# Kernel optimization log

Measured on AMD Instinct MI355X. Metric: run time of the kernel, lower is better.

Reference implementation:

```python
import jax, jax.numpy as jnp
import numpy as np

NDIM = 8
P = NDIM * (NDIM - 1) // 2  # 28 upper-triangular pairs
NHIDDEN = 128
NLAYERS = 3  # first layer + (NLAYERS-1) hidden layers, all followed by softplus
BATCH = 65536


def _pair_indices():
    # torch code iterates j outer, i inner, keeping i < j (i >= j skipped)
    pairs = [(i, j) for j in range(NDIM) for i in range(NDIM) if i < j]
    rel = np.array([[k for k in range(NDIM) if k != i and k != j] for (i, j) in pairs],
                   dtype=np.int32)  # [P, NDIM-2]
    i_idx = np.array([p[0] for p in pairs], dtype=np.int32)
    j_idx = np.array([p[1] for p in pairs], dtype=np.int32)
    return rel, i_idx, j_idx


def setup_inputs() -> dict:
    key = jax.random.key(0)
    ks = jax.random.split(key, 7)
    rel, i_idx, j_idx = _pair_indices()
    d_in = NDIM - 2
    x = jax.random.normal(ks[0], (BATCH, NDIM), dtype=jnp.float32)
    # stacked per-pair MLP parameters (kaiming-ish scale)
    W1 = jax.random.normal(ks[1], (P, d_in, NHIDDEN), dtype=jnp.float32) / np.sqrt(d_in)
    b1 = jax.random.normal(ks[2], (P, NHIDDEN), dtype=jnp.float32) * 0.05
    Wh = jax.random.normal(ks[3], (NLAYERS - 1, P, NHIDDEN, NHIDDEN), dtype=jnp.float32) / np.sqrt(NHIDDEN)
    bh = jax.random.normal(ks[4], (NLAYERS - 1, P, NHIDDEN), dtype=jnp.float32) * 0.05
    Wout = jax.random.normal(ks[5], (P, NHIDDEN), dtype=jnp.float32) / np.sqrt(NHIDDEN)
    bout = jax.random.normal(ks[6], (P,), dtype=jnp.float32) * 0.05
    return {
        "x": x, "W1": W1, "b1": b1, "Wh": Wh, "bh": bh,
        "Wout": Wout, "bout": bout,
        "rel_idx": jnp.asarray(rel), "i_idx": jnp.asarray(i_idx), "j_idx": jnp.asarray(j_idx),
    }


def reference(x, W1, b1, Wh, bh, Wout, bout, rel_idx, i_idx, j_idx):
    # gather the ndim-2 relevant coords for every pair: [B, P, NDIM-2]
    xg = x[:, rel_idx]
    # first linear + softplus (batched over the P pairs)
    h = jax.nn.softplus(jnp.einsum('bpd,pdh->bph', xg, W1) + b1)
    # hidden linears + softplus
    for l in range(Wh.shape[0]):
        h = jax.nn.softplus(jnp.einsum('bph,phk->bpk', h, Wh[l]) + bh[l])
    # output head (no activation): scalar per pair -> [B, P]
    vals = jnp.einsum('bph,ph->bp', h, Wout) + bout
    # scatter into upper triangle, then antisymmetrize
    B = x.shape[0]
    J = jnp.zeros((B, NDIM, NDIM), dtype=x.dtype).at[:, i_idx, j_idx].set(vals)
    return J - jnp.swapaxes(J, 1, 2)
```

## Files before the change

### kernel.cpp

```cpp
#include <hip/hip_runtime.h>

#define NDIM 8
#define P_PAIRS 28
#define HID 128
#define BATCH_N 65536
#define TILE_M 256
#define THREADS 512
#define TILES_PER_BLOCK 4

#define LOG2E 1.4426950408889634f
#define LN2   0.6931471805599453f

typedef __attribute__((ext_vector_type(8))) short bf16x8;
typedef __attribute__((ext_vector_type(4))) float f32x4;

__device__ __forceinline__ unsigned short f32_to_bf16(float f) {
  union { float f; unsigned u; } v; v.f = f;
  unsigned r = v.u + 0x7FFFu + ((v.u >> 16) & 1u);
  return (unsigned short)(r >> 16);
}

__device__ __forceinline__ unsigned cvt_pk_bf16(float a, float b) {
  unsigned r;
  asm("v_cvt_pk_bf16_f32 %0, %1, %2" : "=v"(r) : "v"(a), "v"(b));
  return r;
}

__device__ __forceinline__ float fast_exp2(float x) {
  float r; asm("v_exp_f32 %0, %1" : "=v"(r) : "v"(x)); return r;
}
__device__ __forceinline__ float fast_log2(float x) {
  float r; asm("v_log_f32 %0, %1" : "=v"(r) : "v"(x)); return r;
}

__device__ __forceinline__ float softplus2(float t) {
  t = fminf(t, 126.0f);
  return fast_log2(1.0f + fast_exp2(t));
}

__device__ __forceinline__ int swz(int r, int c8) {
  return r * 128 + (((c8 ^ (r & 15)) & 15) << 3);
}

__global__ void prep_wt(const float* __restrict__ Wh, unsigned short* __restrict__ WT) {
  __shared__ float tile[32][33];
  int t = blockIdx.x;
  int lp = t >> 4;
  int sub = t & 15;
  int kt = (sub >> 2) * 32, nt = (sub & 3) * 32;
  const float* src = Wh + (size_t)lp * 16384;
  unsigned short* dst = WT + (size_t)lp * 16384;
  int tx = threadIdx.x & 31, ty = threadIdx.x >> 5;
#pragma unroll
  for (int r = 0; r < 32; r += 8)
    tile[r + ty][tx] = src[(kt + r + ty) * 128 + (nt + tx)];
  __syncthreads();
#pragma unroll
  for (int r = 0; r < 32; r += 8)
    dst[(nt + r + ty) * 128 + (kt + tx)] = f32_to_bf16(tile[tx][r + ty]);
}

__launch_bounds__(THREADS, 2)
__global__ void mlp_pairs(const float* __restrict__ x,
                          const float* __restrict__ W1,
                          const float* __restrict__ b1,
                          const float* __restrict__ bh,
                          const float* __restrict__ Wout,
                          const float* __restrict__ bout,
                          const int* __restrict__ rel_idx,
                          const int* __restrict__ i_idx,
                          const int* __restrict__ j_idx,
                          const unsigned short* __restrict__ WT,
                          float* __restrict__ out) {
  const int p = blockIdx.y;
  const int bx = blockIdx.x;
  const int tid = (int)threadIdx.x;
  const int lane = tid & 63;
  const int wave = tid >> 6;
  const int qd = lane >> 4;
  const int ln = lane & 15;
  const int mrow = wave * 32;

  __shared__ __align__(16) unsigned short w0_lds[128 * 128];
  __shared__ __align__(16) unsigned short w1_lds[128 * 128];
  __shared__ __align__(16) unsigned short h_lds[TILE_M * 128];
  __shared__ __align__(16) unsigned short xg_lds[TILE_M][8];
  __shared__ __align__(16) unsigned short w1t_lds[128][8];
  __shared__ __align__(16) float b1s[128];
  __shared__ __align__(16) float bh0s[128];
  __shared__ __align__(16) float bh1s[128];
  __shared__ __align__(16) float wouts[128];

  {
    const uint4* s0 = reinterpret_cast<const uint4*>(WT + (size_t)p * 16384);
    const uint4* s1 = reinterpret_cast<const uint4*>(WT + (size_t)(P_PAIRS + p) * 16384);
#pragma unroll
    for (int it = 0; it < 4; ++it) {
      int idx = it * THREADS + tid;
      int r = idx >> 4, c = idx & 15;
      uint4 a = s0[idx];
      uint4 b = s1[idx];
      int off = swz(r, c);
      *reinterpret_cast<uint4*>(&w0_lds[off]) = a;
      *reinterpret_cast<uint4*>(&w1_lds[off]) = b;
    }
  }
  if (tid < 128) {
    int n = tid;
    unsigned short u[8];
#pragma unroll
    for (int k = 0; k < 6; ++k)
      u[k] = f32_to_bf16(W1[(p * 6 + k) * 128 + n] * LOG2E);
    u[6] = 0; u[7] = 0;
    uint4 pk;
    pk.x = (unsigned)u[0] | ((unsigned)u[1] << 16);
    pk.y = (unsigned)u[2] | ((unsigned)u[3] << 16);
    pk.z = (unsigned)u[4] | ((unsigned)u[5] << 16);
    pk.w = 0u;
    *reinterpret_cast<uint4*>(&w1t_lds[n][0]) = pk;
  } else if (tid < 256) {
    int n = tid - 128;
    b1s[n]  = b1[p * 128 + n] * LOG2E;
    bh0s[n] = bh[p * 128 + n] * LOG2E;
    bh1s[n] = bh[(P_PAIRS + p) * 128 + n] * LOG2E;
    wouts[n] = Wout[p * 128 + n] * LN2;
  }
  int rl[6];
#pragma unroll
  for (int d = 0; d < 6; ++d) rl[d] = rel_idx[p * 6 + d];
  const int ii = i_idx[p], jj = j_idx[p];
  const float bp = bout[p];
  __syncthreads();

  float4 xa, xb;
  {
    int row = bx * (TILE_M * TILES_PER_BLOCK) + mrow + (lane & 31);
    const float4* xr = reinterpret_cast<const float4*>(x + (size_t)row * 8);
    if (lane < 32) { xa = xr[0]; xb = xr[1]; }
  }

  for (int itile = 0; itile < TILES_PER_BLOCK; ++itile) {
    const int row0 = bx * (TILE_M * TILES_PER_BLOCK) + itile * TILE_M;

    if (lane < 32) {
      int r = mrow + lane;
      float xv[8] = {xa.x, xa.y, xa.z, xa.w, xb.x, xb.y, xb.z, xb.w};
      unsigned short u[8];
#pragma unroll
      for (int d = 0; d < 6; ++d)
        u[d] = f32_to_bf16(xv[rl[d]]);
      u[6] = 0; u[7] = 0;
      uint4 pk;
      pk.x = (unsigned)u[0] | ((unsigned)u[1] << 16);
      pk.y = (unsigned)u[2] | ((unsigned)u[3] << 16);
      pk.z = (unsigned)u[4] | ((unsigned)u[5] << 16);
      pk.w = 0u;
      *reinterpret_cast<uint4*>(&xg_lds[r][0]) = pk;
    }
    if (itile + 1 < TILES_PER_BLOCK && lane < 32) {
      int row = row0 + TILE_M + mrow + (lane & 31);
      const float4* xr = reinterpret_cast<const float4*>(x + (size_t)row * 8);
      xa = xr[0]; xb = xr[1];
    }

    f32x4 acc[2][8];

#pragma unroll
    for (int nt = 0; nt < 8; ++nt) {
      f32x4 b4 = *reinterpret_cast<const f32x4*>(&b1s[nt * 16 + qd * 4]);
      acc[0][nt] = b4;
      acc[1][nt] = b4;
    }
    {
      bf16x8 zero8 = {};
      bf16x8 bfr[2];
#pragma unroll
      for (int mt = 0; mt < 2; ++mt) {
        bfr[mt] = zero8;
        if (qd == 0)
          bfr[mt] = *reinterpret_cast<const bf16x8*>(&xg_lds[mrow + mt * 16 + ln][0]);
      }
#pragma unroll
      for (int nt = 0; nt < 8; ++nt) {
        bf16x8 afr = zero8;
        if (qd == 0)
          afr = *reinterpret_cast<const bf16x8*>(&w1t_lds[nt * 16 + ln][0]);
#pragma unroll
        for (int mt = 0; mt < 2; ++mt)
          acc[mt][nt] = __builtin_amdgcn_mfma_f32_16x16x32_bf16(afr, bfr[mt], acc[mt][nt], 0, 0, 0);
      }
    }
#pragma unroll
    for (int mt = 0; mt < 2; ++mt) {
      int m = mrow + mt * 16 + ln;
#pragma unroll
      for (int nt = 0; nt < 8; ++nt) {
        uint2 pk;
        pk.x = cvt_pk_bf16(softplus2(acc[mt][nt][0]), softplus2(acc[mt][nt][1]));
        pk.y = cvt_pk_bf16(softplus2(acc[mt][nt][2]), softplus2(acc[mt][nt][3]));
        int off = swz(m, nt * 2 + (qd >> 1)) + (qd & 1) * 4;
        *reinterpret_cast<uint2*>(&h_lds[off]) = pk;
      }
    }

#pragma unroll
    for (int nt = 0; nt < 8; ++nt) {
      f32x4 b4 = *reinterpret_cast<const f32x4*>(&bh0s[nt * 16 + qd * 4]);
      acc[0][nt] = b4;
      acc[1][nt] = b4;
    }
#pragma unroll
    for (int ks = 0; ks < 4; ++ks) {
      bf16x8 bfr[2], afr[8];
#pragma unroll
      for (int mt = 0; mt < 2; ++mt)
        bfr[mt] = *reinterpret_cast<const bf16x8*>(&h_lds[swz(mrow + mt * 16 + ln, ks * 4 + qd)]);
#pragma unroll
      for (int nt = 0; nt < 8; ++nt)
        afr[nt] = *reinterpret_cast<const bf16x8*>(&w0_lds[swz(nt * 16 + ln, ks * 4 + qd)]);
#pragma unroll
      for (int nt = 0; nt < 8; ++nt)
#pragma unroll
        for (int mt = 0; mt < 2; ++mt)
          acc[mt][nt] = __builtin_amdgcn_mfma_f32_16x16x32_bf16(afr[nt], bfr[mt], acc[mt][nt], 0, 0, 0);
    }
#pragma unroll
    for (int mt = 0; mt < 2; ++mt) {
      int m = mrow + mt * 16 + ln;
#pragma unroll
      for (int nt = 0; nt < 8; ++nt) {
        uint2 pk;
        pk.x = cvt_pk_bf16(softplus2(acc[mt][nt][0]), softplus2(acc[mt][nt][1]));
        pk.y = cvt_pk_bf16(softplus2(acc[mt][nt][2]), softplus2(acc[mt][nt][3]));
        int off = swz(m, nt * 2 + (qd >> 1)) + (qd & 1) * 4;
        *reinterpret_cast<uint2*>(&h_lds[off]) = pk;
      }
    }

#pragma unroll
    for (int nt = 0; nt < 8; ++nt) {
      f32x4 b4 = *reinterpret_cast<const f32x4*>(&bh1s[nt * 16 + qd * 4]);
      acc[0][nt] = b4;
      acc[1][nt] = b4;
    }
#pragma unroll
    for (int ks = 0; ks < 4; ++ks) {
      bf16x8 bfr[2], afr[8];
#pragma unroll
      for (int mt = 0; mt < 2; ++mt)
        bfr[mt] = *reinterpret_cast<const bf16x8*>(&h_lds[swz(mrow + mt * 16 + ln, ks * 4 + qd)]);
#pragma unroll
      for (int nt = 0; nt < 8; ++nt)
        afr[nt] = *reinterpret_cast<const bf16x8*>(&w1_lds[swz(nt * 16 + ln, ks * 4 + qd)]);
#pragma unroll
      for (int nt = 0; nt < 8; ++nt)
#pragma unroll
        for (int mt = 0; mt < 2; ++mt)
          acc[mt][nt] = __builtin_amdgcn_mfma_f32_16x16x32_bf16(afr[nt], bfr[mt], acc[mt][nt], 0, 0, 0);
    }
    float pv[2] = {0.f, 0.f};
#pragma unroll
    for (int mt = 0; mt < 2; ++mt) {
#pragma unroll
      for (int nt = 0; nt < 8; ++nt) {
        f32x4 wo4 = *reinterpret_cast<const f32x4*>(&wouts[nt * 16 + qd * 4]);
#pragma unroll
        for (int r = 0; r < 4; ++r)
          pv[mt] += wo4[r] * softplus2(acc[mt][nt][r]);
      }
    }

#pragma unroll
    for (int mt = 0; mt < 2; ++mt) {
      float v = pv[mt];
      v += __shfl_xor(v, 16, 64);
      v += __shfl_xor(v, 32, 64);
      if (lane < 16) {
        int mg = row0 + mrow + mt * 16 + lane;
        float val = v + bp;
        out[mg * 64 + ii * 8 + jj] = val;
        out[mg * 64 + jj * 8 + ii] = -val;
        if (p == 0) {
#pragma unroll
          for (int d = 0; d < 8; ++d)
            out[mg * 64 + d * 9] = 0.f;
        }
      }
    }
  }
}

extern "C" void kernel_launch(void* const* d_in, const int* in_sizes, int n_in,
                              void* d_out, int out_size, void* d_ws, size_t ws_size,
                              hipStream_t stream) {
  const float* x    = (const float*)d_in[0];
  const float* W1   = (const float*)d_in[1];
  const float* b1   = (const float*)d_in[2];
  const float* Wh   = (const float*)d_in[3];
  const float* bh   = (const float*)d_in[4];
  const float* Wout = (const float*)d_in[5];
  const float* bout = (const float*)d_in[6];
  const int* rel    = (const int*)d_in[7];
  const int* iidx   = (const int*)d_in[8];
  const int* jidx   = (const int*)d_in[9];
  float* out = (float*)d_out;
  unsigned short* WT = (unsigned short*)d_ws;

  prep_wt<<<dim3(56 * 16), 256, 0, stream>>>(Wh, WT);
  dim3 grid(BATCH_N / (TILE_M * TILES_PER_BLOCK), P_PAIRS);
  mlp_pairs<<<grid, THREADS, 0, stream>>>(x, W1, b1, bh, Wout, bout, rel, iidx, jidx, WT, out);
}
```

Before: 319.3 us.

## Stagger wave tile order, keep hidden biases in registers, fold bias into first MFMA

Half of the waves now walk their four tiles in a rotated order (starting at tile 2), so different waves sit in different phases (MFMA vs softplus/transcendental) at the same time. Hidden-layer biases are held in registers across tiles and fed as the accumulator input of the first k-step MFMA rather than copied into acc beforehand. Compiler memory fences are placed between stages, and the softplus clamp drops from 126 to 30. Holding the biases costs 64 more VGPRs, which may lower occupancy, and the fences may restrict instruction scheduling.

Result: no change. 322.2 us (+0.9%).

```diff
diff --git a/kernel.cpp b/kernel.cpp
--- a/kernel.cpp
+++ b/kernel.cpp
@@ -14,6 +14,8 @@
 typedef __attribute__((ext_vector_type(8))) short bf16x8;
 typedef __attribute__((ext_vector_type(4))) float f32x4;
 
+#define MEM_FENCE asm volatile("" ::: "memory")
+
 __device__ __forceinline__ unsigned short f32_to_bf16(float f) {
   union { float f; unsigned u; } v; v.f = f;
   unsigned r = v.u + 0x7FFFu + ((v.u >> 16) & 1u);
@@ -34,7 +36,7 @@
 }
 
 __device__ __forceinline__ float softplus2(float t) {
-  t = fminf(t, 126.0f);
+  t = fminf(t, 30.0f);
   return fast_log2(1.0f + fast_exp2(t));
 }
 
@@ -132,14 +134,24 @@
   const float bp = bout[p];
   __syncthreads();
 
-  float4 xa, xb;
+  f32x4 bh0r[8], bh1r[8];
+#pragma unroll
+  for (int nt = 0; nt < 8; ++nt) {
+    bh0r[nt] = *reinterpret_cast<const f32x4*>(&bh0s[nt * 16 + qd * 4]);
+    bh1r[nt] = *reinterpret_cast<const f32x4*>(&bh1s[nt * 16 + qd * 4]);
+  }
+
+  const int phase = (((wave & 1) ^ ((wave >> 2) & 1)) != 0) ? 2 : 0;
+
+  float4 xa = {0.f, 0.f, 0.f, 0.f}, xb = {0.f, 0.f, 0.f, 0.f};
   {
-    int row = bx * (TILE_M * TILES_PER_BLOCK) + mrow + (lane & 31);
+    int row = bx * (TILE_M * TILES_PER_BLOCK) + phase * TILE_M + mrow + (lane & 31);
     const float4* xr = reinterpret_cast<const float4*>(x + (size_t)row * 8);
     if (lane < 32) { xa = xr[0]; xb = xr[1]; }
   }
 
-  for (int itile = 0; itile < TILES_PER_BLOCK; ++itile) {
+  for (int s = 0; s < TILES_PER_BLOCK; ++s) {
+    const int itile = (s + phase) & 3;
     const int row0 = bx * (TILE_M * TILES_PER_BLOCK) + itile * TILE_M;
 
     if (lane < 32) {
@@ -157,20 +169,15 @@
       pk.w = 0u;
       *reinterpret_cast<uint4*>(&xg_lds[r][0]) = pk;
     }
-    if (itile + 1 < TILES_PER_BLOCK && lane < 32) {
-      int row = row0 + TILE_M + mrow + (lane & 31);
-      const float4* xr = reinterpret_cast<const float4*>(x + (size_t)row * 8);
+    MEM_FENCE;
+    if (s + 1 < TILES_PER_BLOCK && lane < 32) {
+      int nrow0 = bx * (TILE_M * TILES_PER_BLOCK) + (((s + 1 + phase) & 3)) * TILE_M;
+      const float4* xr = reinterpret_cast<const float4*>(x + (size_t)(nrow0 + mrow + (lane & 31)) * 8);
       xa = xr[0]; xb = xr[1];
     }
 
     f32x4 acc[2][8];
 
-#pragma unroll
-    for (int nt = 0; nt < 8; ++nt) {
-      f32x4 b4 = *reinterpret_cast<const f32x4*>(&b1s[nt * 16 + qd * 4]);
-      acc[0][nt] = b4;
-      acc[1][nt] = b4;
-    }
     {
       bf16x8 zero8 = {};
       bf16x8 bfr[2];
@@ -185,9 +192,10 @@
         bf16x8 afr = zero8;
         if (qd == 0)
           afr = *reinterpret_cast<const bf16x8*>(&w1t_lds[nt * 16 + ln][0]);
-#pragma unroll
-        for (int mt = 0; mt < 2; ++mt)
-          acc[mt][nt] = __builtin_amdgcn_mfma_f32_16x16x32_bf16(afr, bfr[mt], acc[mt][nt], 0, 0, 0);
+        f32x4 b4 = *reinterpret_cast<const f32x4*>(&b1s[nt * 16 + qd * 4]);
+#pragma unroll
+        for (int mt = 0; mt < 2; ++mt)
+          acc[mt][nt] = __builtin_amdgcn_mfma_f32_16x16x32_bf16(afr, bfr[mt], b4, 0, 0, 0);
       }
     }
 #pragma unroll
@@ -202,15 +210,24 @@
         *reinterpret_cast<uint2*>(&h_lds[off]) = pk;
       }
     }
-
-#pragma unroll
-    for (int nt = 0; nt < 8; ++nt) {
-      f32x4 b4 = *reinterpret_cast<const f32x4*>(&bh0s[nt * 16 + qd * 4]);
-      acc[0][nt] = b4;
-      acc[1][nt] = b4;
-    }
-#pragma unroll
-    for (int ks = 0; ks < 4; ++ks) {
+    MEM_FENCE;
+
+    {
+      bf16x8 bfr[2], afr[8];
+#pragma unroll
+      for (int mt = 0; mt < 2; ++mt)
+        bfr[mt] = *reinterpret_cast<const bf16x8*>(&h_lds[swz(mrow + mt * 16 + ln, qd)]);
+#pragma unroll
+      for (int nt = 0; nt < 8; ++nt)
+        afr[nt] = *reinterpret_cast<const bf16x8*>(&w0_lds[swz(nt * 16 + ln, qd)]);
+#pragma unroll
+      for (int nt = 0; nt < 8; ++nt)
+#pragma unroll
+        for (int mt = 0; mt < 2; ++mt)
+          acc[mt][nt] = __builtin_amdgcn_mfma_f32_16x16x32_bf16(afr[nt], bfr[mt], bh0r[nt], 0, 0, 0);
+    }
+#pragma unroll
+    for (int ks = 1; ks < 4; ++ks) {
       bf16x8 bfr[2], afr[8];
 #pragma unroll
       for (int mt = 0; mt < 2; ++mt)
@@ -236,15 +253,24 @@
         *reinterpret_cast<uint2*>(&h_lds[off]) = pk;
       }
     }
-
-#pragma unroll
-    for (int nt = 0; nt < 8; ++nt) {
-      f32x4 b4 = *reinterpret_cast<const f32x4*>(&bh1s[nt * 16 + qd * 4]);
-      acc[0][nt] = b4;
-      acc[1][nt] = b4;
-    }
-#pragma unroll
-    for (int ks = 0; ks < 4; ++ks) {
+    MEM_FENCE;
+
+    {
+      bf16x8 bfr[2], afr[8];
+#pragma unroll
+      for (int mt = 0; mt < 2; ++mt)
+        bfr[mt] = *reinterpret_cast<const bf16x8*>(&h_lds[swz(mrow + mt * 16 + ln, qd)]);
+#pragma unroll
+      for (int nt = 0; nt < 8; ++nt)
+        afr[nt] = *reinterpret_cast<const bf16x8*>(&w1_lds[swz(nt * 16 + ln, qd)]);
+#pragma unroll
+      for (int nt = 0; nt < 8; ++nt)
+#pragma unroll
+        for (int mt = 0; mt < 2; ++mt)
+          acc[mt][nt] = __builtin_amdgcn_mfma_f32_16x16x32_bf16(afr[nt], bfr[mt], bh1r[nt], 0, 0, 0);
+    }
+#pragma unroll
+    for (int ks = 1; ks < 4; ++ks) {
       bf16x8 bfr[2], afr[8];
 #pragma unroll
       for (int mt = 0; mt < 2; ++mt)
@@ -287,6 +313,7 @@
         }
       }
     }
+    MEM_FENCE;
   }
 }
 
@@ -296,10 +323,10 @@
   const float* x    = (const float*)d_in[0];
   const float* W1   = (const float*)d_in[1];
   const float* b1   = (const float*)d_in[2];
-  const float* Wh   = (const float*)d_in[3];
   const float* bh   = (const float*)d_in[4];
   const float* Wout = (const float*)d_in[5];
   const float* bout = (const float*)d_in[6];
+  const float* Wh   = (const float*)d_in[3];
   const int* rel    = (const int*)d_in[7];
   const int* iidx   = (const int*)d_in[8];
   const int* jidx   = (const int*)d_in[9];
```

## Double block size to sixteen waves with 16-row tiles and staggered tile order

Applied to the files above, without the earlier changes.

Each block now runs 1024 threads. Every wave owns 16 rows instead of 32, which halves the accumulator registers per wave and doubles the waves available to hide MFMA and transcendental latency, since LDS use still limits residency to one block per CU. Bias values are now fed directly as the MFMA initial accumulator. Half the waves start on a different tile (phase offset), with compiler memory fences between stages. The launch bounds now ask for 4 blocks per CU, which may force a very low register cap and cause spills. The softplus clamp is tightened to 30.

Measured after the change: 314.6 us. Within noise of the previous version (-1.5%).

```diff
diff --git a/kernel.cpp b/kernel.cpp
--- a/kernel.cpp
+++ b/kernel.cpp
@@ -5,7 +5,7 @@
 #define HID 128
 #define BATCH_N 65536
 #define TILE_M 256
-#define THREADS 512
+#define THREADS 1024
 #define TILES_PER_BLOCK 4
 
 #define LOG2E 1.4426950408889634f
@@ -13,6 +13,8 @@
 
 typedef __attribute__((ext_vector_type(8))) short bf16x8;
 typedef __attribute__((ext_vector_type(4))) float f32x4;
+
+#define MEM_FENCE asm volatile("" ::: "memory")
 
 __device__ __forceinline__ unsigned short f32_to_bf16(float f) {
   union { float f; unsigned u; } v; v.f = f;
@@ -34,7 +36,7 @@
 }
 
 __device__ __forceinline__ float softplus2(float t) {
-  t = fminf(t, 126.0f);
+  t = fminf(t, 30.0f);
   return fast_log2(1.0f + fast_exp2(t));
 }
 
@@ -60,7 +62,7 @@
     dst[(nt + r + ty) * 128 + (kt + tx)] = f32_to_bf16(tile[tx][r + ty]);
 }
 
-__launch_bounds__(THREADS, 2)
+__launch_bounds__(THREADS, 4)
 __global__ void mlp_pairs(const float* __restrict__ x,
                           const float* __restrict__ W1,
                           const float* __restrict__ b1,
@@ -79,7 +81,7 @@
   const int wave = tid >> 6;
   const int qd = lane >> 4;
   const int ln = lane & 15;
-  const int mrow = wave * 32;
+  const int mrow = wave * 16;
 
   __shared__ __align__(16) unsigned short w0_lds[128 * 128];
   __shared__ __align__(16) unsigned short w1_lds[128 * 128];
@@ -95,7 +97,7 @@
     const uint4* s0 = reinterpret_cast<const uint4*>(WT + (size_t)p * 16384);
     const uint4* s1 = reinterpret_cast<const uint4*>(WT + (size_t)(P_PAIRS + p) * 16384);
 #pragma unroll
-    for (int it = 0; it < 4; ++it) {
+    for (int it = 0; it < 2; ++it) {
       int idx = it * THREADS + tid;
       int r = idx >> 4, c = idx & 15;
       uint4 a = s0[idx];
@@ -132,17 +134,20 @@
   const float bp = bout[p];
   __syncthreads();
 
-  float4 xa, xb;
+  const int phase = ((wave >> 2) & 1) * 2;
+
+  float4 xa = {0.f, 0.f, 0.f, 0.f}, xb = {0.f, 0.f, 0.f, 0.f};
   {
-    int row = bx * (TILE_M * TILES_PER_BLOCK) + mrow + (lane & 31);
+    int row = bx * (TILE_M * TILES_PER_BLOCK) + phase * TILE_M + mrow + ln;
     const float4* xr = reinterpret_cast<const float4*>(x + (size_t)row * 8);
-    if (lane < 32) { xa = xr[0]; xb = xr[1]; }
+    if (lane < 16) { xa = xr[0]; xb = xr[1]; }
   }
 
-  for (int itile = 0; itile < TILES_PER_BLOCK; ++itile) {
+  for (int s = 0; s < TILES_PER_BLOCK; ++s) {
+    const int itile = (s + phase) & 3;
     const int row0 = bx * (TILE_M * TILES_PER_BLOCK) + itile * TILE_M;
 
-    if (lane < 32) {
+    if (lane < 16) {
       int r = mrow + lane;
       float xv[8] = {xa.x, xa.y, xa.z, xa.w, xb.x, xb.y, xb.z, xb.w};
       unsigned short u[8];
@@ -157,126 +162,110 @@
       pk.w = 0u;
       *reinterpret_cast<uint4*>(&xg_lds[r][0]) = pk;
     }
-    if (itile + 1 < TILES_PER_BLOCK && lane < 32) {
-      int row = row0 + TILE_M + mrow + (lane & 31);
-      const float4* xr = reinterpret_cast<const float4*>(x + (size_t)row * 8);
+    MEM_FENCE;
+    if (s + 1 < TILES_PER_BLOCK && lane < 16) {
+      int nrow0 = bx * (TILE_M * TILES_PER_BLOCK) + (((s + 1 + phase) & 3)) * TILE_M;
+      const float4* xr = reinterpret_cast<const float4*>(x + (size_t)(nrow0 + mrow + ln) * 8);
       xa = xr[0]; xb = xr[1];
     }
 
-    f32x4 acc[2][8];
-
-#pragma unroll
-    for (int nt = 0; nt < 8; ++nt) {
-      f32x4 b4 = *reinterpret_cast<const f32x4*>(&b1s[nt * 16 + qd * 4]);
-      acc[0][nt] = b4;
-      acc[1][nt] = b4;
-    }
+    f32x4 acc[8];
+
     {
       bf16x8 zero8 = {};
-      bf16x8 bfr[2];
-#pragma unroll
-      for (int mt = 0; mt < 2; ++mt) {
-        bfr[mt] = zero8;
-        if (qd == 0)
-          bfr[mt] = *reinterpret_cast<const bf16x8*>(&xg_lds[mrow + mt * 16 + ln][0]);
-      }
+      bf16x8 bfr = zero8;
+      if (qd == 0)
+        bfr = *reinterpret_cast<const bf16x8*>(&xg_lds[mrow + ln][0]);
 #pragma unroll
       for (int nt = 0; nt < 8; ++nt) {
         bf16x8 afr = zero8;
         if (qd == 0)
           afr = *reinterpret_cast<const bf16x8*>(&w1t_lds[nt * 16 + ln][0]);
-#pragma unroll
-        for (int mt = 0; mt < 2; ++mt)
-          acc[mt][nt] = __builtin_amdgcn_mfma_f32_16x16x32_bf16(afr, bfr[mt], acc[mt][nt], 0, 0, 0);
-      }
-    }
-#pragma unroll
-    for (int mt = 0; mt < 2; ++mt) {
-      int m = mrow + mt * 16 + ln;
+        f32x4 b4 = *reinterpret_cast<const f32x4*>(&b1s[nt * 16 + qd * 4]);
+        acc[nt] = __builtin_amdgcn_mfma_f32_16x16x32_bf16(afr, bfr, b4, 0, 0, 0);
+      }
+    }
+    {
+      int m = mrow + ln;
 #pragma unroll
       for (int nt = 0; nt < 8; ++nt) {
         uint2 pk;
-        pk.x = cvt_pk_bf16(softplus2(acc[mt][nt][0]), softplus2(acc[mt][nt][1]));
-        pk.y = cvt_pk_bf16(softplus2(acc[mt][nt][2]), softplus2(acc[mt][nt][3]));
+        pk.x = cvt_pk_bf16(softplus2(acc[nt][0]), softplus2(acc[nt][1]));
+        pk.y = cvt_pk_bf16(softplus2(acc[nt][2]), softplus2(acc[nt][3]));
         int off = swz(m, nt * 2 + (qd >> 1)) + (qd & 1) * 4;
         *reinterpret_cast<uint2*>(&h_lds[off]) = pk;
       }
     }
-
-#pragma unroll
-    for (int nt = 0; nt < 8; ++nt) {
-      f32x4 b4 = *reinterpret_cast<const f32x4*>(&bh0s[nt * 16 + qd * 4]);
-      acc[0][nt] = b4;
-      acc[1][nt] = b4;
-    }
-#pragma unroll
-    for (int ks = 0; ks < 4; ++ks) {
-      bf16x8 bfr[2], afr[8];
-#pragma unroll
-      for (int mt = 0; mt < 2; ++mt)
-        bfr[mt] = *reinterpret_cast<const bf16x8*>(&h_lds[swz(mrow + mt * 16 + ln, ks * 4 + qd)]);
+    MEM_FENCE;
+
+    {
+      bf16x8 bfr = *reinterpret_cast<const bf16x8*>(&h_lds[swz(mrow + ln, qd)]);
+#pragma unroll
+      for (int nt = 0; nt < 8; ++nt) {
+        bf16x8 afr = *reinterpret_cast<const bf16x8*>(&w0_lds[swz(nt * 16 + ln, qd)]);
+        f32x4 b4 = *reinterpret_cast<const f32x4*>(&bh0s[nt * 16 + qd * 4]);
+        acc[nt] = __builtin_amdgcn_mfma_f32_16x16x32_bf16(afr, bfr, b4, 0, 0, 0);
+      }
+    }
+#pragma unroll
+    for (int ks = 1; ks < 4; ++ks) {
+      bf16x8 bfr = *reinterpret_cast<const bf16x8*>(&h_lds[swz(mrow + ln, ks * 4 + qd)]);
+      bf16x8 afr[8];
 #pragma unroll
       for (int nt = 0; nt < 8; ++nt)
         afr[nt] = *reinterpret_cast<const bf16x8*>(&w0_lds[swz(nt * 16 + ln, ks * 4 + qd)]);
 #pragma unroll
       for (int nt = 0; nt < 8; ++nt)
-#pragma unroll
-        for (int mt = 0; mt < 2; ++mt)
-          acc[mt][nt] = __builtin_amdgcn_mfma_f32_16x16x32_bf16(afr[nt], bfr[mt], acc[mt][nt], 0, 0, 0);
-    }
-#pragma unroll
-    for (int mt = 0; mt < 2; ++mt) {
-      int m = mrow + mt * 16 + ln;
+        acc[nt] = __builtin_amdgcn_mfma_f32_16x16x32_bf16(afr[nt], bfr, acc[nt], 0, 0, 0);
+    }
+    {
+      int m = mrow + ln;
 #pragma unroll
       for (int nt = 0; nt < 8; ++nt) {
         uint2 pk;
-        pk.x = cvt_pk_bf16(softplus2(acc[mt][nt][0]), softplus2(acc[mt][nt][1]));
-        pk.y = cvt_pk_bf16(softplus2(acc[mt][nt][2]), softplus2(acc[mt][nt][3]));
+        pk.x = cvt_pk_bf16(softplus2(acc[nt][0]), softplus2(acc[nt][1]));
+        pk.y = cvt_pk_bf16(softplus2(acc[nt][2]), softplus2(acc[nt][3]));
         int off = swz(m, nt * 2 + (qd >> 1)) + (qd & 1) * 4;
         *reinterpret_cast<uint2*>(&h_lds[off]) = pk;
       }
     }
-
-#pragma unroll
-    for (int nt = 0; nt < 8; ++nt) {
-      f32x4 b4 = *reinterpret_cast<const f32x4*>(&bh1s[nt * 16 + qd * 4]);
-      acc[0][nt] = b4;
-      acc[1][nt] = b4;
-    }
-#pragma unroll
-    for (int ks = 0; ks < 4; ++ks) {
-      bf16x8 bfr[2], afr[8];
-#pragma unroll
-      for (int mt = 0; mt < 2; ++mt)
-        bfr[mt] = *reinterpret_cast<const bf16x8*>(&h_lds[swz(mrow + mt * 16 + ln, ks * 4 + qd)]);
+    MEM_FENCE;
+
+    {
+      bf16x8 bfr = *reinterpret_cast<const bf16x8*>(&h_lds[swz(mrow + ln, qd)]);
+#pragma unroll
+      for (int nt = 0; nt < 8; ++nt) {
+        bf16x8 afr = *reinterpret_cast<const bf16x8*>(&w1_lds[swz(nt * 16 + ln, qd)]);
+        f32x4 b4 = *reinterpret_cast<const f32x4*>(&bh1s[nt * 16 + qd * 4]);
+        acc[nt] = __builtin_amdgcn_mfma_f32_16x16x32_bf16(afr, bfr, b4, 0, 0, 0);
+      }
+    }
+#pragma unroll
+    for (int ks = 1; ks < 4; ++ks) {
+      bf16x8 bfr = *reinterpret_cast<const bf16x8*>(&h_lds[swz(mrow + ln, ks * 4 + qd)]);
+      bf16x8 afr[8];
 #pragma unroll
       for (int nt = 0; nt < 8; ++nt)
         afr[nt] = *reinterpret_cast<const bf16x8*>(&w1_lds[swz(nt * 16 + ln, ks * 4 + qd)]);
 #pragma unroll
       for (int nt = 0; nt < 8; ++nt)
-#pragma unroll
-        for (int mt = 0; mt < 2; ++mt)
-          acc[mt][nt] = __builtin_amdgcn_mfma_f32_16x16x32_bf16(afr[nt], bfr[mt], acc[mt][nt], 0, 0, 0);
-    }
-    float pv[2] = {0.f, 0.f};
-#pragma unroll
-    for (int mt = 0; mt < 2; ++mt) {
-#pragma unroll
-      for (int nt = 0; nt < 8; ++nt) {
-        f32x4 wo4 = *reinterpret_cast<const f32x4*>(&wouts[nt * 16 + qd * 4]);
-#pragma unroll
-        for (int r = 0; r < 4; ++r)
-          pv[mt] += wo4[r] * softplus2(acc[mt][nt][r]);
-      }
-    }
-
-#pragma unroll
-    for (int mt = 0; mt < 2; ++mt) {
-      float v = pv[mt];
+        acc[nt] = __builtin_amdgcn_mfma_f32_16x16x32_bf16(afr[nt], bfr, acc[nt], 0, 0, 0);
+    }
+    float pv = 0.f;
+#pragma unroll
+    for (int nt = 0; nt < 8; ++nt) {
+      f32x4 wo4 = *reinterpret_cast<const f32x4*>(&wouts[nt * 16 + qd * 4]);
+#pragma unroll
+      for (int r = 0; r < 4; ++r)
+        pv += wo4[r] * softplus2(acc[nt][r]);
+    }
+
+    {
+      float v = pv;
       v += __shfl_xor(v, 16, 64);
       v += __shfl_xor(v, 32, 64);
       if (lane < 16) {
-        int mg = row0 + mrow + mt * 16 + lane;
+        int mg = row0 + mrow + lane;
         float val = v + bp;
         out[mg * 64 + ii * 8 + jj] = val;
         out[mg * 64 + jj * 8 + ii] = -val;
@@ -287,6 +276,7 @@
         }
       }
     }
+    MEM_FENCE;
   }
 }
 
```
